# Kernel optimization log

Measured on AMD Instinct MI355X. Metric: run time of the kernel, lower is better.

## Reference

```python
import jax, jax.numpy as jnp
import numpy as np

# Token-layout constants from the module
NOTE_ON_START = 0
NOTE_OFF_START = 128
TIME_SHIFT_START = 256
VELOCITY_START = 768
RHYTHM_W = 1.0
HARMONY_W = 1.0
VOICE_W = 0.5


def setup_inputs() -> dict:
    key = jax.random.key(0)
    B, S = 512, 16384
    tokens = jax.random.randint(key, (B, S), 0, 774, dtype=jnp.int64)
    return {"generated_tokens": tokens}


def _prev_masked_index(mask):
    # For each position t, index of the most recent masked position strictly before t
    # within the same row; -1 if none. mask: [B, S] bool.
    B, S = mask.shape
    pos = jnp.arange(S, dtype=jnp.int32)[None, :]
    p = jnp.where(mask, pos, -1)
    run_max = jax.lax.cummax(p, axis=1)  # last masked index <= t
    prev = jnp.concatenate(
        [jnp.full((B, 1), -1, dtype=run_max.dtype), run_max[:, :-1]], axis=1
    )
    return prev, pos


def reference(generated_tokens):
    tokens = generated_tokens
    B, S = tokens.shape
    f32 = jnp.float32

    # ---------------- rhythm regularity ----------------
    time_mask = (tokens >= TIME_SHIFT_START) & (tokens < VELOCITY_START)
    prev_t, pos = _prev_masked_index(time_mask)
    valid_t = time_mask & (prev_t >= 0)  # each masked pos with a predecessor in its row
    diffs = (pos - prev_t).astype(f32)   # position gaps (only meaningful where valid_t)
    w = valid_t.astype(f32)
    n = jnp.sum(w)
    sum_d = jnp.sum(diffs * w)
    mean = sum_d / jnp.maximum(n, 1.0)
    # unbiased variance (torch.var default, ddof=1)
    ss = jnp.sum(w * (diffs - mean) ** 2)
    var = jnp.where(n > 1.0, ss / jnp.maximum(n - 1.0, 1.0), 0.0)
    rhythm = var * 0.01

    # ---------------- harmony consistency ----------------
    note_mask = (tokens >= NOTE_ON_START) & (tokens < NOTE_OFF_START)
    pc = tokens % 12  # pitch class
    pair = note_mask[:, :-1] & note_mask[:, 1:]
    tritone = jnp.abs(pc[:, :-1] - pc[:, 1:]) == 6
    harmony = 0.1 * jnp.sum((pair & tritone).astype(f32)) / f32(B * S)

    # ---------------- voice leading ----------------
    prev_n, _ = _prev_masked_index(note_mask)
    prev_val = jnp.take_along_axis(tokens, jnp.maximum(prev_n, 0).astype(jnp.int64), axis=1)
    valid_n = note_mask & (prev_n >= 0)
    interval = (tokens - prev_val).astype(f32)
    leaps = valid_n & (jnp.abs(interval) > 12.0)
    voice = jnp.sum(leaps.astype(f32)) / f32(B)

    total = RHYTHM_W * rhythm + HARMONY_W * harmony + VOICE_W * voice
    # [rhythm_constraint, harmony_constraint, voice_leading_constraint, total]
    return jnp.stack([rhythm, harmony, voice, total])
```

## Files before the change

### kernel.cpp

```cpp
#include <hip/hip_runtime.h>


#define BATCH 512
#define SEQ   16384
#define TPB   1024
#define EPT   (SEQ / TPB)
#define NWAVES (TPB / 64)
#define LDS_DW (SEQ + (SEQ >> 4) + 1)

__global__ __launch_bounds__(TPB) void
mcl_scan_kernel(const int* __restrict__ tokens,
                int* __restrict__ ct_a, int* __restrict__ sd_a,
                int* __restrict__ sd2_a, int* __restrict__ harm_a,
                int* __restrict__ leap_a)
{
    const int row  = blockIdx.x;
    const int t    = threadIdx.x;
    const int lane = t & 63;
    const int wave = t >> 6;

    __shared__ int s_tok[LDS_DW];
    __shared__ int s_time[NWAVES];
    __shared__ int s_note[NWAVES];
    __shared__ int s_red[NWAVES][6];

    const int4* v4 = (const int4*)(tokens + (size_t)row * SEQ);

    int4 x[4];
#pragma unroll
    for (int c = 0; c < 4; ++c) x[c] = v4[c * TPB + t];
#pragma unroll
    for (int c = 0; c < 4; ++c) {
        const int u = c * TPB + t;
        const int bdw = 17 * (u >> 2) + 4 * (u & 3);
        s_tok[bdw + 0] = x[c].x; s_tok[bdw + 1] = x[c].y;
        s_tok[bdw + 2] = x[c].z; s_tok[bdw + 3] = x[c].w;
    }
    __syncthreads();

    const int rbase = 17 * t;
    int n_time = 0, sd2 = 0, harm = 0, leaps = 0;
    int first_time = 0x7FFFFFFF, last_time = -1;
    int first_note_val = -1, last_note_pos = -1, last_note_val = 0;

#pragma unroll
    for (int j = 0; j < EPT; ++j) {
        const int tok = s_tok[rbase + j];
        const int pos = (t << 4) + j;
        const bool is_time = (unsigned)(tok - 256) < 512u;
        const bool is_note = (unsigned)tok < 128u;
        if (is_time) {
            if (last_time >= 0) {
                const int d = pos - last_time;
                sd2 += d * d;
            } else first_time = pos;
            last_time = pos;
            n_time++;
        }
        if (is_note) {
            if (last_note_pos >= 0) {
                if ((unsigned)(tok - last_note_val + 12) > 24u) leaps++;
            } else first_note_val = tok;
            last_note_pos = pos; last_note_val = tok;
        }
        const int nb = (j < EPT - 1) ? s_tok[rbase + j + 1]
                                     : ((t < TPB - 1) ? s_tok[rbase + 17] : -1);
        if (is_note && (unsigned)nb < 128u) {
            const unsigned u = (unsigned)(tok - nb + 126);
            const unsigned q = (u * 43691u) >> 19;
            if (q * 12u == u) harm++;
        }
    }

    int note_pack = (last_note_pos >= 0) ? ((last_note_pos << 10) | last_note_val) : -1;
    int lt = last_time, np = note_pack;
#pragma unroll
    for (int off = 1; off < 64; off <<= 1) {
        int a = __shfl_up(lt, off);
        int b = __shfl_up(np, off);
        if (lane >= off) { lt = max(lt, a); np = max(np, b); }
    }
    int excl_t = __shfl_up(lt, 1);
    int excl_n = __shfl_up(np, 1);
    if (lane == 0) { excl_t = -1; excl_n = -1; }
    if (lane == 63) { s_time[wave] = lt; s_note[wave] = np; }
    __syncthreads();
    int pt = -1, pn = -1;
    for (int w = 0; w < wave; ++w) {
        pt = max(pt, s_time[w]);
        pn = max(pn, s_note[w]);
    }
    const int prev_time = max(pt, excl_t);
    const int prev_note = max(pn, excl_n);

    if (first_time != 0x7FFFFFFF && prev_time >= 0) {
        const int d = first_time - prev_time;
        sd2 += d * d;
    }
    if (first_note_val >= 0 && prev_note >= 0) {
        if ((unsigned)(first_note_val - (prev_note & 1023) + 12) > 24u) leaps++;
    }

#pragma unroll
    for (int off = 32; off; off >>= 1) {
        n_time += __shfl_down(n_time, off);
        sd2    += __shfl_down(sd2, off);
        harm   += __shfl_down(harm, off);
        leaps  += __shfl_down(leaps, off);
        first_time = min(first_time, __shfl_down(first_time, off));
    }
    if (lane == 0) {
        s_red[wave][0] = n_time; s_red[wave][1] = sd2;
        s_red[wave][2] = harm;   s_red[wave][3] = leaps;
        s_red[wave][4] = first_time;
    }
    __syncthreads();
    if (t == 0) {
        int a0 = 0, a1 = 0, a2 = 0, a3 = 0, fmin = 0x7FFFFFFF, lmax = -1;
        for (int w = 0; w < NWAVES; ++w) {
            a0 += s_red[w][0]; a1 += s_red[w][1];
            a2 += s_red[w][2]; a3 += s_red[w][3];
            fmin = min(fmin, s_red[w][4]);
            lmax = max(lmax, s_time[w]);
        }
        ct_a[row]   = (a0 > 0) ? (a0 - 1) : 0;
        sd_a[row]   = (a0 > 0) ? (lmax - fmin) : 0;
        sd2_a[row]  = a1;
        harm_a[row] = a2;
        leap_a[row] = a3;
    }
}

__global__ __launch_bounds__(512) void
mcl_final_kernel(const int* __restrict__ ct_a, const int* __restrict__ sd_a,
                 const int* __restrict__ sd2_a, const int* __restrict__ harm_a,
                 const int* __restrict__ leap_a, float* __restrict__ out)
{
    const int t = threadIdx.x;
    const int lane = t & 63, wave = t >> 6;
    long long v0 = ct_a[t], v1 = sd_a[t], v2 = sd2_a[t];
    long long v3 = harm_a[t], v4 = leap_a[t];
#pragma unroll
    for (int off = 32; off; off >>= 1) {
        v0 += __shfl_down(v0, off);
        v1 += __shfl_down(v1, off);
        v2 += __shfl_down(v2, off);
        v3 += __shfl_down(v3, off);
        v4 += __shfl_down(v4, off);
    }
    __shared__ long long s[8][5];
    if (lane == 0) { s[wave][0]=v0; s[wave][1]=v1; s[wave][2]=v2; s[wave][3]=v3; s[wave][4]=v4; }
    __syncthreads();
    if (t == 0) {
        long long A = 0, Bs = 0, C = 0, D = 0, E = 0;
        for (int w = 0; w < 8; ++w) { A+=s[w][0]; Bs+=s[w][1]; C+=s[w][2]; D+=s[w][3]; E+=s[w][4]; }
        const double n = (double)A;
        double rhythm = 0.0;
        if (A > 1) {
            const double ss = (double)C - ((double)Bs * (double)Bs) / n;
            rhythm = 0.01 * ss / (n - 1.0);
        }
        const double harmony = 0.1 * (double)D / ((double)BATCH * (double)SEQ);
        const double voice   = (double)E / (double)BATCH;
        out[0] = (float)rhythm;
        out[1] = (float)harmony;
        out[2] = (float)voice;
        out[3] = (float)(rhythm + harmony + 0.5 * voice);
    }
}

extern "C" void kernel_launch(void* const* d_in, const int* in_sizes, int n_in,
                              void* d_out, int out_size, void* d_ws, size_t ws_size,
                              hipStream_t stream)
{
    const int* tokens = (const int*)d_in[0];
    float* out = (float*)d_out;

    char* ws = (char*)d_ws;
    int* ct_a   = (int*)ws;
    int* sd_a   = (int*)(ws + 2048);
    int* sd2_a  = (int*)(ws + 4096);
    int* harm_a = (int*)(ws + 6144);
    int* leap_a = (int*)(ws + 8192);

    mcl_scan_kernel<<<BATCH, TPB, 0, stream>>>(tokens, ct_a, sd_a, sd2_a, harm_a, leap_a);
    mcl_final_kernel<<<1, 512, 0, stream>>>(ct_a, sd_a, sd2_a, harm_a, leap_a, out);
}
```

Measured before the change: 82.27 us.

## Split each row into four segment blocks and stitch boundaries in final kernel

```diff
diff --git a/kernel.cpp b/kernel.cpp
--- a/kernel.cpp
+++ b/kernel.cpp
@@ -3,35 +3,40 @@
 
 #define BATCH 512
 #define SEQ   16384
-#define TPB   1024
-#define EPT   (SEQ / TPB)
+#define TPB   256
+#define EPT   16
+#define SEG   (TPB * EPT)
+#define SEGS  (SEQ / SEG)
 #define NWAVES (TPB / 64)
-#define LDS_DW (SEQ + (SEQ >> 4) + 1)
+#define LDS_DW (SEG + (SEG >> 4) + 1)
 
 __global__ __launch_bounds__(TPB) void
-mcl_scan_kernel(const int* __restrict__ tokens,
-                int* __restrict__ ct_a, int* __restrict__ sd_a,
-                int* __restrict__ sd2_a, int* __restrict__ harm_a,
-                int* __restrict__ leap_a)
+mcl_scan_kernel(const int* __restrict__ tokens, int* __restrict__ seg_out)
 {
-    const int row  = blockIdx.x;
+    const int blk  = blockIdx.x;
+    const int row  = blk >> 2;
+    const int seg  = blk & 3;
     const int t    = threadIdx.x;
     const int lane = t & 63;
     const int wave = t >> 6;
 
     __shared__ int s_tok[LDS_DW];
+    __shared__ int s_halo;
     __shared__ int s_time[NWAVES];
     __shared__ int s_note[NWAVES];
-    __shared__ int s_red[NWAVES][6];
-
-    const int4* v4 = (const int4*)(tokens + (size_t)row * SEQ);
+    __shared__ int s_red[NWAVES][8];
+
+    const int* rowp  = tokens + (size_t)row * SEQ;
+    const int  gbase = seg * SEG;
+    const int4* v4   = (const int4*)(rowp + gbase);
 
     int4 x[4];
 #pragma unroll
     for (int c = 0; c < 4; ++c) x[c] = v4[c * TPB + t];
+    if (t == 0) s_halo = (seg < SEGS - 1) ? rowp[gbase + SEG] : -1;
 #pragma unroll
     for (int c = 0; c < 4; ++c) {
-        const int u = c * TPB + t;
+        const int u   = c * TPB + t;
         const int bdw = 17 * (u >> 2) + 4 * (u & 3);
         s_tok[bdw + 0] = x[c].x; s_tok[bdw + 1] = x[c].y;
         s_tok[bdw + 2] = x[c].z; s_tok[bdw + 3] = x[c].w;
@@ -39,14 +44,16 @@
     __syncthreads();
 
     const int rbase = 17 * t;
+    const int pbase = gbase + (t << 4);
     int n_time = 0, sd2 = 0, harm = 0, leaps = 0;
     int first_time = 0x7FFFFFFF, last_time = -1;
-    int first_note_val = -1, last_note_pos = -1, last_note_val = 0;
+    int first_note_pack = 0x7FFFFFFF;
+    int last_note_pos = -1, last_note_val = 0;
 
 #pragma unroll
     for (int j = 0; j < EPT; ++j) {
         const int tok = s_tok[rbase + j];
-        const int pos = (t << 4) + j;
+        const int pos = pbase + j;
         const bool is_time = (unsigned)(tok - 256) < 512u;
         const bool is_note = (unsigned)tok < 128u;
         if (is_time) {
@@ -60,11 +67,11 @@
         if (is_note) {
             if (last_note_pos >= 0) {
                 if ((unsigned)(tok - last_note_val + 12) > 24u) leaps++;
-            } else first_note_val = tok;
+            } else first_note_pack = (pos << 10) | tok;
             last_note_pos = pos; last_note_val = tok;
         }
         const int nb = (j < EPT - 1) ? s_tok[rbase + j + 1]
-                                     : ((t < TPB - 1) ? s_tok[rbase + 17] : -1);
+                     : ((t < TPB - 1) ? s_tok[rbase + 17] : s_halo);
         if (is_note && (unsigned)nb < 128u) {
             const unsigned u = (unsigned)(tok - nb + 126);
             const unsigned q = (u * 43691u) >> 19;
@@ -97,8 +104,8 @@
         const int d = first_time - prev_time;
         sd2 += d * d;
     }
-    if (first_note_val >= 0 && prev_note >= 0) {
-        if ((unsigned)(first_note_val - (prev_note & 1023) + 12) > 24u) leaps++;
+    if (first_note_pack != 0x7FFFFFFF && prev_note >= 0) {
+        if ((unsigned)((first_note_pack & 1023) - (prev_note & 1023) + 12) > 24u) leaps++;
     }
 
 #pragma unroll
@@ -107,39 +114,68 @@
         sd2    += __shfl_down(sd2, off);
         harm   += __shfl_down(harm, off);
         leaps  += __shfl_down(leaps, off);
-        first_time = min(first_time, __shfl_down(first_time, off));
+        first_time      = min(first_time, __shfl_down(first_time, off));
+        first_note_pack = min(first_note_pack, __shfl_down(first_note_pack, off));
     }
     if (lane == 0) {
         s_red[wave][0] = n_time; s_red[wave][1] = sd2;
         s_red[wave][2] = harm;   s_red[wave][3] = leaps;
         s_red[wave][4] = first_time;
+        s_red[wave][5] = first_note_pack;
     }
     __syncthreads();
     if (t == 0) {
-        int a0 = 0, a1 = 0, a2 = 0, a3 = 0, fmin = 0x7FFFFFFF, lmax = -1;
+        int a0 = 0, a1 = 0, a2 = 0, a3 = 0;
+        int ftm = 0x7FFFFFFF, fnp = 0x7FFFFFFF, ltm = -1, lnp = -1;
         for (int w = 0; w < NWAVES; ++w) {
             a0 += s_red[w][0]; a1 += s_red[w][1];
             a2 += s_red[w][2]; a3 += s_red[w][3];
-            fmin = min(fmin, s_red[w][4]);
-            lmax = max(lmax, s_time[w]);
-        }
-        ct_a[row]   = (a0 > 0) ? (a0 - 1) : 0;
-        sd_a[row]   = (a0 > 0) ? (lmax - fmin) : 0;
-        sd2_a[row]  = a1;
-        harm_a[row] = a2;
-        leap_a[row] = a3;
+            ftm = min(ftm, s_red[w][4]);
+            fnp = min(fnp, s_red[w][5]);
+            ltm = max(ltm, s_time[w]);
+            lnp = max(lnp, s_note[w]);
+        }
+        int* o = seg_out + blk * 8;
+        o[0] = a0; o[1] = a1; o[2] = a2; o[3] = a3;
+        o[4] = ftm; o[5] = ltm; o[6] = fnp; o[7] = lnp;
     }
 }
 
 __global__ __launch_bounds__(512) void
-mcl_final_kernel(const int* __restrict__ ct_a, const int* __restrict__ sd_a,
-                 const int* __restrict__ sd2_a, const int* __restrict__ harm_a,
-                 const int* __restrict__ leap_a, float* __restrict__ out)
+mcl_final_kernel(const int* __restrict__ seg_out, float* __restrict__ out)
 {
     const int t = threadIdx.x;
     const int lane = t & 63, wave = t >> 6;
-    long long v0 = ct_a[t], v1 = sd_a[t], v2 = sd2_a[t];
-    long long v3 = harm_a[t], v4 = leap_a[t];
+
+    const int* p = seg_out + t * (SEGS * 8);
+    int n_time = 0, sd2 = 0, harm = 0, leaps = 0;
+    int run_last_t = -1, run_last_np = -1;
+    int row_first_t = 0x7FFFFFFF;
+#pragma unroll
+    for (int s = 0; s < SEGS; ++s) {
+        const int nt  = p[s*8+0], s2  = p[s*8+1];
+        const int hm  = p[s*8+2], lp  = p[s*8+3];
+        const int ftm = p[s*8+4], ltm = p[s*8+5];
+        const int fnp = p[s*8+6], lnp = p[s*8+7];
+        n_time += nt; sd2 += s2; harm += hm; leaps += lp;
+        if (nt > 0) {
+            if (run_last_t >= 0) {
+                const int d = ftm - run_last_t;
+                sd2 += d * d;
+            } else row_first_t = ftm;
+            run_last_t = ltm;
+        }
+        if (fnp != 0x7FFFFFFF) {
+            if (run_last_np >= 0) {
+                if ((unsigned)((fnp & 1023) - (run_last_np & 1023) + 12) > 24u) leaps++;
+            }
+            run_last_np = lnp;
+        }
+    }
+    long long v0 = (n_time > 0) ? (n_time - 1) : 0;
+    long long v1 = (n_time > 0) ? (run_last_t - row_first_t) : 0;
+    long long v2 = sd2, v3 = harm, v4 = leaps;
+
 #pragma unroll
     for (int off = 32; off; off >>= 1) {
         v0 += __shfl_down(v0, off);
@@ -175,14 +211,8 @@
 {
     const int* tokens = (const int*)d_in[0];
     float* out = (float*)d_out;
-
-    char* ws = (char*)d_ws;
-    int* ct_a   = (int*)ws;
-    int* sd_a   = (int*)(ws + 2048);
-    int* sd2_a  = (int*)(ws + 4096);
-    int* harm_a = (int*)(ws + 6144);
-    int* leap_a = (int*)(ws + 8192);
-
-    mcl_scan_kernel<<<BATCH, TPB, 0, stream>>>(tokens, ct_a, sd_a, sd2_a, harm_a, leap_a);
-    mcl_final_kernel<<<1, 512, 0, stream>>>(ct_a, sd_a, sd2_a, harm_a, leap_a, out);
+    int* seg_out = (int*)d_ws;
+
+    mcl_scan_kernel<<<BATCH * SEGS, TPB, 0, stream>>>(tokens, seg_out);
+    mcl_final_kernel<<<1, BATCH, 0, stream>>>(seg_out, out);
 }
```

Measured after the change: 82.25 us. About the same (-0.0%).
